# Performance work log

Measured on AMD Instinct MI355X. Metric: run time of the kernel, lower is better.

The kernel has to match this reference:

```python
import jax, jax.numpy as jnp
import numpy as np

B, L, D = 4, 2048, 768
K, M, CK = 12, 1, 4            # heads, thetas, conv kernel size
H = D // (K * M)               # 64
DIM_MEM = K * H                # 768
DIM_EXPAND = H * 3             # 192
DSH = DIM_EXPAND * 2           # 384 swiglu head dim
DST = K * DSH                  # 4608
DIM_FUSED = DIM_MEM + K + DST  # 5388
THETA_MIN, THETA_MAX = 1e-3, 3.0


def setup_inputs() -> dict:
    key = jax.random.key(0)
    ks = jax.random.split(key, 5)
    x = jax.random.normal(ks[0], (B, L, D), jnp.float32)
    W_in = jax.random.normal(ks[1], (D, DIM_FUSED), jnp.float32) * 0.02
    conv_w = jax.random.normal(ks[2], (CK, DIM_MEM + K), jnp.float32) * 0.2  # depthwise taps
    rms_scale = jnp.ones((H,), jnp.float32)
    # theta_raw init (M==1 branch): inverse-sigmoid of geomspace grid
    grid = np.geomspace(THETA_MIN, THETA_MAX, K).reshape(1, 1, K, 1, 1)
    base = np.tile(grid, (1, 1, 1, H, 1))
    u = np.clip((base - THETA_MIN) / (THETA_MAX - THETA_MIN), 1e-4, 1 - 1e-4)
    theta_raw = jnp.asarray(np.log(u) - np.log(1.0 - u), jnp.float32)
    decay_slopes = jnp.asarray(np.log(np.exp(np.geomspace(1e-3, 0.1, K)) - 1.0), jnp.float32)
    score_scale = jnp.ones((K,), jnp.float32)
    tanh_scale = jnp.ones((K,), jnp.float32)
    W_sw = jax.random.normal(ks[3], (2 * K * H * M, DST), jnp.float32) * 0.02
    W_out = jax.random.normal(ks[4], (K * DIM_EXPAND, D), jnp.float32) * 0.02
    return {"x": x, "W_in": W_in, "conv_w": conv_w, "rms_scale": rms_scale,
            "theta_raw": theta_raw, "decay_slopes": decay_slopes,
            "score_scale": score_scale, "tanh_scale": tanh_scale,
            "W_sw": W_sw, "W_out": W_out}


def reference(x, W_in, conv_w, rms_scale, theta_raw, decay_slopes,
              score_scale, tanh_scale, W_sw, W_out):
    # fused in-projection
    z_fused = jnp.einsum('bld,df->blf', x, W_in)
    z_mem = z_fused[..., :DIM_MEM + K]
    skip_direct = z_fused[..., DIM_MEM + K:]
    # causal depthwise conv (kernel size CK, left pad CK-1)
    zp = jnp.pad(z_mem, ((0, 0), (CK - 1, 0), (0, 0)))
    z_conv = sum(zp[:, j:j + L, :] * conv_w[j] for j in range(CK))
    z_mem = jax.nn.silu(z_conv)
    # memory keys + RMSNorm over H
    k_val = z_mem[..., :DIM_MEM].reshape(B, L, K, H)
    k_val = k_val * jax.lax.rsqrt(jnp.mean(k_val * k_val, axis=-1, keepdims=True) + 1e-6) * rms_scale
    s_raw = z_mem[..., DIM_MEM:]  # (B, L, K)
    # theta (M == 1)
    theta = THETA_MIN + (THETA_MAX - THETA_MIN) * jax.nn.sigmoid(theta_raw)  # (1,1,K,H,1)
    # decay time weights (num_anchor_heads == 0, maxlen == L)
    pos = jnp.arange(L, dtype=jnp.float32)
    slopes = jax.nn.softplus(decay_slopes).reshape(1, 1, K)
    dist = jnp.maximum(jnp.float32(L - 1) - pos, 0.0)
    log_time_weight = -slopes * dist[None, :, None]  # (1, L, K)
    log_p = jnp.clip(score_scale[None, None, :] * s_raw, -10.0, 10.0)
    p_w = jnp.exp(log_p + log_time_weight)  # (B, L, K)
    # characteristic-function encoding
    k5 = k_val[..., None]  # (B, L, K, H, 1)
    phi = jnp.tanh(k5 * tanh_scale.reshape(1, 1, K, 1, 1)) * theta
    kvw = k5 * p_w[..., None, None]
    re = kvw * jnp.cos(phi)
    im = kvw * jnp.sin(phi)
    # fused causal cumulative accumulation
    flat = K * H * M
    stack = jnp.concatenate([p_w, re.reshape(B, L, flat), im.reshape(B, L, flat)], axis=-1)
    cs = jnp.cumsum(stack, axis=1)
    den_acc = cs[..., :K]
    re_acc = cs[..., K:K + flat].reshape(B, L, K, H, M)
    im_acc = cs[..., K + flat:].reshape(B, L, K, H, M)
    inv_den = (1.0 / jnp.maximum(den_acc, 1e-4))[..., None, None]
    summary_flat = jnp.stack([re_acc * inv_den, im_acc * inv_den], axis=-1).reshape(B, L, -1)
    # SwiGLU with skip
    y_spectral = jnp.einsum('bls,sf->blf', summary_flat, W_sw).reshape(B, L, K, DSH)
    y_skip = skip_direct.reshape(B, L, K, DSH)
    y_spec_val, y_spec_gate = jnp.split(y_spectral, 2, axis=-1)
    y_skip_val, y_skip_gate = jnp.split(y_skip, 2, axis=-1)
    y_act = (y_spec_val + y_skip_val) * jax.nn.silu(y_spec_gate + y_skip_gate)
    out = jnp.einsum('blf,fd->bld', y_act.reshape(B, L, -1), W_out)
    return out
```

## Files before the change

kernel.cpp:

```cpp
#include <hip/hip_runtime.h>
#include <hip/hip_bf16.h>

#define B_       4
#define L_       2048
#define D_       768
#define K_       12
#define H_       64
#define CK_      4
#define DIM_MEM_ 768
#define DMK      780
#define NT       (B_*L_)
#define NSUM     1536
#define NACT     2304
#define NCHUNK   16
#define CHLEN    (L_/NCHUNK)
#define PSTRIDE  132

typedef __attribute__((ext_vector_type(8))) short          bf16x8;
typedef __attribute__((ext_vector_type(8))) unsigned short u16x8;
typedef __attribute__((ext_vector_type(4))) float          f32x4;

__device__ __forceinline__ ushort f2bf(float v) {
    __hip_bfloat16 h = __float2bfloat16(v);
    return *reinterpret_cast<ushort*>(&h);
}
__device__ __forceinline__ float tanh_fast(float x) {
    float t = __expf(-2.f * fabsf(x));
    float r = (1.f - t) / (1.f + t);
    return copysignf(r, x);
}

struct PrepJobs {
    const float* W[6];
    ushort*      out[6];
    int ldw[6], Kd[6], colbase[6], remap[6], ntx[6];
    int start[7];
    const float* cast_in;
    ushort*      cast_out;
    int n4;
};

__global__ __launch_bounds__(256)
void prep_all(PrepJobs J)
{
    int blk = blockIdx.x;
    if (blk >= J.start[6]) {
        int i = (blk - J.start[6]) * 256 + threadIdx.x;
        if (i < J.n4) {
            float4 v = reinterpret_cast<const float4*>(J.cast_in)[i];
            ushort4 o;
            o.x = f2bf(v.x); o.y = f2bf(v.y); o.z = f2bf(v.z); o.w = f2bf(v.w);
            reinterpret_cast<ushort4*>(J.cast_out)[i] = o;
        }
        return;
    }
    int j = 0;
    while (blk >= J.start[j + 1]) ++j;
    int rel = blk - J.start[j];
    int ntx = J.ntx[j];
    int n0 = (rel % ntx) * 32, k0 = (rel / ntx) * 32;
    const float* W = J.W[j];
    int ldw = J.ldw[j], Kd = J.Kd[j], colbase = J.colbase[j], remap = J.remap[j];
    ushort* out = J.out[j];

    __shared__ float tile[32][33];
    int tx = threadIdx.x & 31, ty = threadIdx.x >> 5;
    int n = n0 + tx;
    int c;
    if (remap) {
        int grp = n >> 5, which = (n >> 4) & 1, nn = (grp << 4) + (n & 15);
        c = colbase + (nn / 192) * 384 + which * 192 + (nn % 192);
    } else {
        c = colbase + n;
    }
    #pragma unroll
    for (int r = 0; r < 4; ++r)
        tile[ty + r*8][tx] = W[(size_t)(k0 + ty + r*8) * ldw + c];
    __syncthreads();
    #pragma unroll
    for (int r = 0; r < 4; ++r)
        out[(size_t)(n0 + ty + r*8) * Kd + k0 + tx] = f2bf(tile[tx][ty + r*8]);
}

__global__ __launch_bounds__(256)
void gemm_bf16_mfma(const ushort* __restrict__ A, const ushort* __restrict__ BT,
                    float* __restrict__ C, int Kd, int N, int ldc)
{
    __shared__ ushort As[128*64];
    __shared__ ushort Bs[128*64];
    int tid = threadIdx.x, lane = tid & 63;
    int lr = lane & 15, quad = lane >> 4;
    int wave = tid >> 6;
    int wr = (wave >> 1) * 64, wc = (wave & 1) * 64;
    int m0 = blockIdx.y * 128, n0 = blockIdx.x * 128;

    f32x4 acc[4][4] = {};

    int srow = tid >> 3;
    int tc   = tid & 7;
    const ushort* gA = A  + (size_t)(m0 + srow) * Kd + tc * 8;
    const ushort* gB = BT + (size_t)(n0 + srow) * Kd + tc * 8;
    int woff = srow * 64 + ((tc ^ (srow & 7)) * 8);
    int rx = lr & 7;

    for (int k0 = 0; k0 < Kd; k0 += 64) {
        u16x8 a[4], b[4];
        #pragma unroll
        for (int p = 0; p < 4; ++p) {
            a[p] = *reinterpret_cast<const u16x8*>(gA + (size_t)(32*p) * Kd);
            b[p] = *reinterpret_cast<const u16x8*>(gB + (size_t)(32*p) * Kd);
        }
        gA += 64; gB += 64;
        __syncthreads();
        #pragma unroll
        for (int p = 0; p < 4; ++p) {
            *reinterpret_cast<u16x8*>(As + woff + p*2048) = a[p];
            *reinterpret_cast<u16x8*>(Bs + woff + p*2048) = b[p];
        }
        __syncthreads();
        #pragma unroll
        for (int ks = 0; ks < 2; ++ks) {
            bf16x8 af[4], bf[4];
            #pragma unroll
            for (int i = 0; i < 4; ++i) {
                int ca = ((ks*4 + quad) ^ rx) * 8;
                af[i] = *reinterpret_cast<const bf16x8*>(As + (wr + i*16 + lr) * 64 + ca);
                bf[i] = *reinterpret_cast<const bf16x8*>(Bs + (wc + i*16 + lr) * 64 + ca);
            }
            #pragma unroll
            for (int i = 0; i < 4; ++i)
                #pragma unroll
                for (int j = 0; j < 4; ++j)
                    acc[i][j] = __builtin_amdgcn_mfma_f32_16x16x32_bf16(
                                    af[i], bf[j], acc[i][j], 0, 0, 0);
        }
    }

    #pragma unroll
    for (int i = 0; i < 4; ++i)
        #pragma unroll
        for (int j = 0; j < 4; ++j)
            #pragma unroll
            for (int r = 0; r < 4; ++r) {
                int row = m0 + wr + i*16 + quad*4 + r;
                int col = n0 + wc + j*16 + lr;
                if (col < N)
                    C[(size_t)row * ldc + col] = acc[i][j][r];
            }
}

#define G2NKT 36

#define GLOAD16(gp, dp) __builtin_amdgcn_global_load_lds( \
    (__attribute__((address_space(1))) const void*)(gp),  \
    (__attribute__((address_space(3))) void*)(dp), 16, 0, 0)

__device__ __forceinline__ void g2_stageA(ushort* lds_, int kt,
                                          const ushort* pAs, const ushort* pAx,
                                          int wave, int part)
{
    int ktc = kt > (G2NKT-1) ? (G2NKT-1) : kt;
    const ushort* g; size_t kd;
    if (ktc < 24) { g = pAs + ktc*64;      kd = 1536; }
    else          { g = pAx + (ktc-24)*64; kd = 768;  }
    g += (size_t)(part * 64) * kd;
    ushort* d = lds_ + (kt & 1) * 8192 + part * 4096 + wave * 512;
    GLOAD16(g,           d);
    GLOAD16(g + 32*kd,   d + 2048);
}

__device__ __forceinline__ void g2_stageB(ushort* lds_, int kt,
                                          const ushort* pBs, const ushort* pBx,
                                          int wave)
{
    int ktc = kt > (G2NKT-1) ? (G2NKT-1) : kt;
    const ushort* g; size_t kd;
    if (ktc < 24) { g = pBs + ktc*64;      kd = 1536; }
    else          { g = pBx + (ktc-24)*64; kd = 768;  }
    ushort* d = lds_ + 16384 + (kt & 1) * 12288 + wave * 512;
    #pragma unroll
    for (int s = 0; s < 6; ++s)
        GLOAD16(g + (size_t)(32*s)*kd, d + 2048*s);
}

__global__ __launch_bounds__(256, 2)
void gemm2_1ph(const ushort* __restrict__ Sm, const ushort* __restrict__ Xb,
               const ushort* __restrict__ WsC, const ushort* __restrict__ WiC,
               ushort* __restrict__ yact)
{
    __shared__ ushort lds[40960];
    const int tid  = threadIdx.x;
    const int lane = tid & 63, wave = tid >> 6;
    const int lr = lane & 15, quad = lane >> 4, rx = lr & 7;
    const int wr = (wave >> 1) * 64;
    const int wc = (wave & 1) * 96;
    const int m0 = blockIdx.y * 128, n0 = blockIdx.x * 192;

    const int sr = tid >> 3;
    const int sc = (tid & 7) ^ (sr & 7);
    const ushort* pAs = Sm  + (size_t)(m0 + sr) * 1536 + sc * 8;
    const ushort* pAx = Xb  + (size_t)(m0 + sr) * 768  + sc * 8;
    const ushort* pBs = WsC + (size_t)(n0 + sr) * 1536 + sc * 8;
    const ushort* pBx = WiC + (size_t)(n0 + sr) * 768  + sc * 8;

    f32x4 acc[4][6] = {};
    const int ca0 = (quad ^ rx) * 8;
    const int ca1 = ((4 + quad) ^ rx) * 8;

    g2_stageA(lds, 0, pAs, pAx, wave, 0);
    g2_stageA(lds, 0, pAs, pAx, wave, 1);
    g2_stageB(lds, 0, pBs, pBx, wave);
    asm volatile("s_waitcnt vmcnt(0)" ::: "memory");
    __builtin_amdgcn_s_barrier();

    #pragma unroll 1
    for (int g = 0; g < G2NKT; ++g) {
        const ushort* Ab = lds + (g & 1) * 8192;
        const ushort* Bb = lds + 16384 + (g & 1) * 12288;

        g2_stageA(lds, g + 1, pAs, pAx, wave, 0);
        g2_stageA(lds, g + 1, pAs, pAx, wave, 1);
        g2_stageB(lds, g + 1, pBs, pBx, wave);

        bf16x8 af[4][2], bfr[6][2];
        #pragma unroll
        for (int i = 0; i < 4; ++i) {
            const ushort* p = Ab + (wr + i*16 + lr) * 64;
            af[i][0] = *reinterpret_cast<const bf16x8*>(p + ca0);
            af[i][1] = *reinterpret_cast<const bf16x8*>(p + ca1);
        }
        #pragma unroll
        for (int j = 0; j < 6; ++j) {
            const ushort* p = Bb + (wc + j*16 + lr) * 64;
            bfr[j][0] = *reinterpret_cast<const bf16x8*>(p + ca0);
            bfr[j][1] = *reinterpret_cast<const bf16x8*>(p + ca1);
        }
        __builtin_amdgcn_s_setprio(1);
        #pragma unroll
        for (int ks = 0; ks < 2; ++ks)
            #pragma unroll
            for (int i = 0; i < 4; ++i)
                #pragma unroll
                for (int j = 0; j < 6; ++j)
                    acc[i][j] = __builtin_amdgcn_mfma_f32_16x16x32_bf16(
                                    af[i][ks], bfr[j][ks], acc[i][j], 0, 0, 0);
        __builtin_amdgcn_s_setprio(0);

        asm volatile("s_waitcnt vmcnt(0)" ::: "memory");
        __builtin_amdgcn_s_barrier();
    }

    const int vg0 = (n0 + wc) >> 5;
    #pragma unroll
    for (int i = 0; i < 4; ++i)
        #pragma unroll
        for (int p = 0; p < 3; ++p)
            #pragma unroll
            for (int r = 0; r < 4; ++r) {
                int row = m0 + wr + i*16 + quad*4 + r;
                int col = (vg0 + p)*16 + lr;
                float v  = acc[i][2*p][r];
                float gt = acc[i][2*p + 1][r];
                float y = v * (gt / (1.f + __expf(-gt)));
                yact[(size_t)row * NACT + col] = f2bf(y);
            }
}

__global__ __launch_bounds__(256)
void token_kernel(const float* __restrict__ zmem, const float* __restrict__ conv_w,
                  const float* __restrict__ rms_scale, const float* __restrict__ theta_raw,
                  const float* __restrict__ dslopes, const float* __restrict__ sscale,
                  const float* __restrict__ tscale,
                  float* __restrict__ pw, float* __restrict__ re, float* __restrict__ im)
{
    int t = blockIdx.x;
    int b = t >> 11;
    int l = t & (L_ - 1);
    int tid = threadIdx.x;
    int h = tid & 63, kg = tid >> 6;

    __shared__ float s_pw[K_];

    if (tid < K_) {
        float acc = 0.f;
        #pragma unroll
        for (int j = 0; j < CK_; ++j) {
            int ll = l - (CK_ - 1) + j;
            if (ll >= 0)
                acc += zmem[(size_t)(b*L_ + ll)*DMK + DIM_MEM_ + tid]
                     * conv_w[j*DMK + DIM_MEM_ + tid];
        }
        float s  = acc / (1.f + expf(-acc));
        float lp = sscale[tid] * s;
        lp = fminf(10.f, fmaxf(-10.f, lp));
        float slope = log1pf(expf(dslopes[tid]));
        s_pw[tid] = expf(lp - slope * (float)(L_ - 1 - l));
    }

    float kv[3];
    #pragma unroll
    for (int q = 0; q < 3; ++q) {
        int kk = kg + q*4;
        int c = kk*H_ + h;
        float acc = 0.f;
        #pragma unroll
        for (int j = 0; j < CK_; ++j) {
            int ll = l - (CK_ - 1) + j;
            if (ll >= 0)
                acc += zmem[(size_t)(b*L_ + ll)*DMK + c] * conv_w[j*DMK + c];
        }
        kv[q] = acc / (1.f + __expf(-acc));
    }
    __syncthreads();

    #pragma unroll
    for (int q = 0; q < 3; ++q) {
        int kk = kg + q*4;
        float v = kv[q];
        float ss = v * v;
        #pragma unroll
        for (int off = 32; off > 0; off >>= 1)
            ss += __shfl_xor(ss, off, 64);
        float kn = v * rsqrtf(ss * (1.f/64.f) + 1e-6f) * rms_scale[h];
        float th = 0.001f + 2.999f * (1.f / (1.f + __expf(-theta_raw[kk*H_ + h])));
        float phi = tanh_fast(kn * tscale[kk]) * th;
        float kvw = kn * s_pw[kk];
        re[(size_t)t*(K_*H_) + kk*H_ + h] = kvw * __cosf(phi);
        im[(size_t)t*(K_*H_) + kk*H_ + h] = kvw * __sinf(phi);
    }
    if (tid < K_) pw[(size_t)t*K_ + tid] = s_pw[tid];
}

__global__ __launch_bounds__(128)
void scan_sums(const float* __restrict__ pw, const float* __restrict__ re,
               const float* __restrict__ im, float* __restrict__ part)
{
    int blk = blockIdx.x;
    int chunk = blk & (NCHUNK - 1);
    int bk = blk >> 4;
    int k = bk % K_;
    int b = bk / K_;
    int tid = threadIdx.x;
    int h = tid & 63;
    const float* __restrict__ src = (tid >> 6) ? im : re;
    int l0 = chunk * CHLEN;

    size_t base  = ((size_t)(b*L_ + l0))*(K_*H_) + k*H_ + h;
    size_t dbase = ((size_t)(b*L_ + l0))*K_ + k;
    float s = 0.f, ds = 0.f;
    for (int i0 = 0; i0 < CHLEN; i0 += 8) {
        float v[8], d[8];
        #pragma unroll
        for (int j = 0; j < 8; ++j) {
            v[j] = src[base + (size_t)(i0 + j)*(K_*H_)];
            d[j] = pw [dbase + (size_t)(i0 + j)*K_];
        }
        #pragma unroll
        for (int j = 0; j < 8; ++j) { s += v[j]; ds += d[j]; }
    }
    size_t pb = ((size_t)bk * NCHUNK + chunk) * PSTRIDE;
    part[pb + tid] = s;
    if (tid == 0) part[pb + 128] = ds;
}

__global__ __launch_bounds__(128)
void scan_final(const float* __restrict__ pw, const float* __restrict__ re,
                const float* __restrict__ im, const float* __restrict__ part,
                ushort* __restrict__ summary)
{
    int blk = blockIdx.x;
    int chunk = blk & (NCHUNK - 1);
    int bk = blk >> 4;
    int k = bk % K_;
    int b = bk / K_;
    int tid = threadIdx.x;
    int h = tid & 63;
    int pi = tid >> 6;
    const float* __restrict__ src = pi ? im : re;
    int l0 = chunk * CHLEN;

    float acc = 0.f, dacc = 0.f;
    size_t pb0 = (size_t)bk * NCHUNK * PSTRIDE;
    for (int cn = 0; cn < chunk; ++cn) {
        acc  += part[pb0 + (size_t)cn*PSTRIDE + tid];
        dacc += part[pb0 + (size_t)cn*PSTRIDE + 128];
    }

    size_t base  = ((size_t)(b*L_ + l0))*(K_*H_) + k*H_ + h;
    size_t dbase = ((size_t)(b*L_ + l0))*K_ + k;
    int outch = 2*(k*H_ + h) + pi;
    for (int i0 = 0; i0 < CHLEN; i0 += 8) {
        float v[8], d[8];
        #pragma unroll
        for (int j = 0; j < 8; ++j) {
            v[j] = src[base + (size_t)(i0 + j)*(K_*H_)];
            d[j] = pw [dbase + (size_t)(i0 + j)*K_];
        }
        #pragma unroll
        for (int j = 0; j < 8; ++j) {
            acc += v[j]; dacc += d[j];
            float inv = 1.f / fmaxf(dacc, 1e-4f);
            summary[((size_t)(b*L_ + l0 + i0 + j))*NSUM + outch] = f2bf(acc * inv);
        }
    }
}

extern "C" void kernel_launch(void* const* d_in, const int* in_sizes, int n_in,
                              void* d_out, int out_size, void* d_ws, size_t ws_size,
                              hipStream_t stream)
{
    const float* x         = (const float*)d_in[0];
    const float* W_in      = (const float*)d_in[1];
    const float* conv_w    = (const float*)d_in[2];
    const float* rms_scale = (const float*)d_in[3];
    const float* theta_raw = (const float*)d_in[4];
    const float* dslopes   = (const float*)d_in[5];
    const float* sscale    = (const float*)d_in[6];
    const float* tscale    = (const float*)d_in[7];
    const float* W_sw      = (const float*)d_in[8];
    const float* W_out     = (const float*)d_in[9];
    float* out = (float*)d_out;
    char* ws   = (char*)d_ws;

    float*  zmem    = (float*) (ws + 0);
    ushort* summary = (ushort*)(ws + 0);
    float*  pw      = (float*) (ws + 25559040);
    float*  re      = (float*) (ws + 25952256);
    float*  im      = (float*) (ws + 51118080);
    ushort* yact    = (ushort*)(ws + 25952256);
    float*  part    = (float*) (ws + 76283904);
    ushort* xb      = (ushort*)(ws + 76689408);
    ushort* WiCat   = (ushort*)(ws + 89272320);
    ushort* WsCat   = (ushort*)(ws + 96350208);
    ushort* WoT     = (ushort*)(ws + 110505984);
    ushort* WimT    = (ushort*)(ws + 114044928);

    PrepJobs J{};
    J.W[0]=W_in;  J.out[0]=WiCat; J.ldw[0]=5388; J.Kd[0]=768;  J.colbase[0]=780; J.remap[0]=1; J.ntx[0]=144;
    J.W[1]=W_sw;  J.out[1]=WsCat; J.ldw[1]=4608; J.Kd[1]=1536; J.colbase[1]=0;   J.remap[1]=1; J.ntx[1]=144;
    J.W[2]=W_out; J.out[2]=WoT;   J.ldw[2]=768;  J.Kd[2]=2304; J.colbase[2]=0;   J.remap[2]=0; J.ntx[2]=24;
    J.W[3]=W_in;  J.out[3]=WimT;  J.ldw[3]=5388; J.Kd[3]=768;  J.colbase[3]=0;   J.remap[3]=0; J.ntx[3]=28;
    int tiles[4] = {144*24, 144*48, 24*72, 28*24};
    J.start[0] = 0;
    for (int j = 0; j < 4; ++j) J.start[j+1] = J.start[j] + tiles[j];
    J.start[5] = J.start[4];
    J.start[6] = J.start[4];
    J.cast_in = x; J.cast_out = xb; J.n4 = NT*D_/4;
    int nblk = J.start[6] + (J.n4 + 255)/256;

    dim3 blk(256);
    prep_all<<<dim3(nblk), blk, 0, stream>>>(J);
    gemm_bf16_mfma<<<dim3(7, 64), blk, 0, stream>>>(xb, WimT, zmem, 768, 780, 780);
    token_kernel<<<dim3(NT), blk, 0, stream>>>(zmem, conv_w, rms_scale, theta_raw,
                                               dslopes, sscale, tscale, pw, re, im);
    scan_sums <<<dim3(B_*K_*NCHUNK), dim3(128), 0, stream>>>(pw, re, im, part);
    scan_final<<<dim3(B_*K_*NCHUNK), dim3(128), 0, stream>>>(pw, re, im, part, summary);
    gemm2_1ph<<<dim3(24, 64), dim3(256), 0, stream>>>(summary, xb, WsCat, WiCat, yact);
    gemm_bf16_mfma<<<dim3(6, 64), blk, 0, stream>>>(yact, WoT, out, 2304, 768, 768);
}
```

Before: 418.3 us.

## Load GEMM2 A operand directly into registers, staging only B through LDS

The second GEMM no longer stages the A tile (summary/x rows) through shared memory. Each wave loads its own A fragments straight from global memory into double-buffered registers one k-step ahead, and only B goes through LDS via global_load_lds. The loop is unrolled by two with alternating register buffers, and the wait only drains the B LDS loads (vmcnt(8)), so the A register loads stay in flight. This shrinks LDS from 80KB to 48KB and removes the A LDS reads, at the cost of more VGPRs and less coalesced global reads, since each lane reads 16 bytes from separate rows.

```diff
diff --git a/kernel.cpp b/kernel.cpp
--- a/kernel.cpp
+++ b/kernel.cpp
@@ -149,46 +149,58 @@
             }
 }
 
-#define G2NKT 36
-
 #define GLOAD16(gp, dp) __builtin_amdgcn_global_load_lds( \
     (__attribute__((address_space(1))) const void*)(gp),  \
     (__attribute__((address_space(3))) void*)(dp), 16, 0, 0)
 
-__device__ __forceinline__ void g2_stageA(ushort* lds_, int kt,
-                                          const ushort* pAs, const ushort* pAx,
-                                          int wave, int part)
-{
-    int ktc = kt > (G2NKT-1) ? (G2NKT-1) : kt;
-    const ushort* g; size_t kd;
-    if (ktc < 24) { g = pAs + ktc*64;      kd = 1536; }
-    else          { g = pAx + (ktc-24)*64; kd = 768;  }
-    g += (size_t)(part * 64) * kd;
-    ushort* d = lds_ + (kt & 1) * 8192 + part * 4096 + wave * 512;
-    GLOAD16(g,           d);
-    GLOAD16(g + 32*kd,   d + 2048);
-}
-
-__device__ __forceinline__ void g2_stageB(ushort* lds_, int kt,
-                                          const ushort* pBs, const ushort* pBx,
-                                          int wave)
-{
-    int ktc = kt > (G2NKT-1) ? (G2NKT-1) : kt;
-    const ushort* g; size_t kd;
-    if (ktc < 24) { g = pBs + ktc*64;      kd = 1536; }
-    else          { g = pBx + (ktc-24)*64; kd = 768;  }
-    ushort* d = lds_ + 16384 + (kt & 1) * 12288 + wave * 512;
-    #pragma unroll
-    for (int s = 0; s < 6; ++s)
-        GLOAD16(g + (size_t)(32*s)*kd, d + 2048*s);
-}
+#define G2BODY(AF_USE, AF_LD, PAR, PREF, PA_NEXT, KDA, PB_NEXT, KDB)          \
+  do {                                                                        \
+    if (PREF) {                                                               \
+        ushort* bd = lds + ((PAR)^1)*12288 + wave*512;                        \
+        const ushort* bsrc = (PB_NEXT);                                       \
+        _Pragma("unroll")                                                     \
+        for (int s = 0; s < 6; ++s)                                           \
+            GLOAD16(bsrc + (size_t)(32*s)*(KDB), bd + 2048*s);                \
+        __builtin_amdgcn_sched_barrier(0);   \
+        const ushort* asrc = (PA_NEXT);                                       \
+        _Pragma("unroll")                                                     \
+        for (int i = 0; i < 4; ++i) {                                         \
+            AF_LD[i][0] = *reinterpret_cast<const bf16x8*>(                   \
+                              asrc + (size_t)(i*16)*(KDA));                   \
+            AF_LD[i][1] = *reinterpret_cast<const bf16x8*>(                   \
+                              asrc + (size_t)(i*16)*(KDA) + 32);              \
+        }                                                                     \
+    }                                                                         \
+    const ushort* Bb = lds + (PAR)*12288;                                     \
+    bf16x8 bfr[6][2];                                                         \
+    _Pragma("unroll")                                                         \
+    for (int j = 0; j < 6; ++j) {                                             \
+        const ushort* p = Bb + (wc + j*16 + lr) * 64;                         \
+        bfr[j][0] = *reinterpret_cast<const bf16x8*>(p + ca0);                \
+        bfr[j][1] = *reinterpret_cast<const bf16x8*>(p + ca1);                \
+    }                                                                         \
+    __builtin_amdgcn_s_setprio(1);                                            \
+    _Pragma("unroll")                                                         \
+    for (int ks = 0; ks < 2; ++ks)                                            \
+        _Pragma("unroll")                                                     \
+        for (int i = 0; i < 4; ++i)                                           \
+            _Pragma("unroll")                                                 \
+            for (int j = 0; j < 6; ++j)                                       \
+                acc[i][j] = __builtin_amdgcn_mfma_f32_16x16x32_bf16(          \
+                                AF_USE[i][ks], bfr[j][ks], acc[i][j], 0,0,0); \
+    __builtin_amdgcn_s_setprio(0);                                            \
+    if (PREF) {                                                               \
+        asm volatile("s_waitcnt vmcnt(8)" ::: "memory");                      \
+        __builtin_amdgcn_s_barrier();                                         \
+    }                                                                         \
+  } while (0)
 
 __global__ __launch_bounds__(256, 2)
-void gemm2_1ph(const ushort* __restrict__ Sm, const ushort* __restrict__ Xb,
-               const ushort* __restrict__ WsC, const ushort* __restrict__ WiC,
-               ushort* __restrict__ yact)
-{
-    __shared__ ushort lds[40960];
+void gemm2_areg(const ushort* __restrict__ Sm, const ushort* __restrict__ Xb,
+                const ushort* __restrict__ WsC, const ushort* __restrict__ WiC,
+                ushort* __restrict__ yact)
+{
+    __shared__ ushort lds[24576];
     const int tid  = threadIdx.x;
     const int lane = tid & 63, wave = tid >> 6;
     const int lr = lane & 15, quad = lane >> 4, rx = lr & 7;
@@ -198,57 +210,46 @@
 
     const int sr = tid >> 3;
     const int sc = (tid & 7) ^ (sr & 7);
-    const ushort* pAs = Sm  + (size_t)(m0 + sr) * 1536 + sc * 8;
-    const ushort* pAx = Xb  + (size_t)(m0 + sr) * 768  + sc * 8;
-    const ushort* pBs = WsC + (size_t)(n0 + sr) * 1536 + sc * 8;
-    const ushort* pBx = WiC + (size_t)(n0 + sr) * 768  + sc * 8;
+    const ushort* pB1 = WsC + (size_t)(n0 + sr) * 1536 + sc * 8;
+    const ushort* pB2 = WiC + (size_t)(n0 + sr) * 768  + sc * 8;
+
+    const ushort* pA1 = Sm + (size_t)(m0 + wr + lr) * 1536 + quad * 8;
+    const ushort* pA2 = Xb + (size_t)(m0 + wr + lr) * 768  + quad * 8;
 
     f32x4 acc[4][6] = {};
+    bf16x8 af0[4][2], af1[4][2];
     const int ca0 = (quad ^ rx) * 8;
     const int ca1 = ((4 + quad) ^ rx) * 8;
 
-    g2_stageA(lds, 0, pAs, pAx, wave, 0);
-    g2_stageA(lds, 0, pAs, pAx, wave, 1);
-    g2_stageB(lds, 0, pBs, pBx, wave);
-    asm volatile("s_waitcnt vmcnt(0)" ::: "memory");
-    __builtin_amdgcn_s_barrier();
+    {
+        ushort* bd = lds + wave*512;
+        #pragma unroll
+        for (int s = 0; s < 6; ++s)
+            GLOAD16(pB1 + (size_t)(32*s)*1536, bd + 2048*s);
+        __builtin_amdgcn_sched_barrier(0);
+        #pragma unroll
+        for (int i = 0; i < 4; ++i) {
+            af0[i][0] = *reinterpret_cast<const bf16x8*>(pA1 + (size_t)(i*16)*1536);
+            af0[i][1] = *reinterpret_cast<const bf16x8*>(pA1 + (size_t)(i*16)*1536 + 32);
+        }
+        asm volatile("s_waitcnt vmcnt(8)" ::: "memory");
+        __builtin_amdgcn_s_barrier();
+    }
 
     #pragma unroll 1
-    for (int g = 0; g < G2NKT; ++g) {
-        const ushort* Ab = lds + (g & 1) * 8192;
-        const ushort* Bb = lds + 16384 + (g & 1) * 12288;
-
-        g2_stageA(lds, g + 1, pAs, pAx, wave, 0);
-        g2_stageA(lds, g + 1, pAs, pAx, wave, 1);
-        g2_stageB(lds, g + 1, pBs, pBx, wave);
-
-        bf16x8 af[4][2], bfr[6][2];
-        #pragma unroll
-        for (int i = 0; i < 4; ++i) {
-            const ushort* p = Ab + (wr + i*16 + lr) * 64;
-            af[i][0] = *reinterpret_cast<const bf16x8*>(p + ca0);
-            af[i][1] = *reinterpret_cast<const bf16x8*>(p + ca1);
-        }
-        #pragma unroll
-        for (int j = 0; j < 6; ++j) {
-            const ushort* p = Bb + (wc + j*16 + lr) * 64;
-            bfr[j][0] = *reinterpret_cast<const bf16x8*>(p + ca0);
-            bfr[j][1] = *reinterpret_cast<const bf16x8*>(p + ca1);
-        }
-        __builtin_amdgcn_s_setprio(1);
-        #pragma unroll
-        for (int ks = 0; ks < 2; ++ks)
-            #pragma unroll
-            for (int i = 0; i < 4; ++i)
-                #pragma unroll
-                for (int j = 0; j < 6; ++j)
-                    acc[i][j] = __builtin_amdgcn_mfma_f32_16x16x32_bf16(
-                                    af[i][ks], bfr[j][ks], acc[i][j], 0, 0, 0);
-        __builtin_amdgcn_s_setprio(0);
-
-        asm volatile("s_waitcnt vmcnt(0)" ::: "memory");
-        __builtin_amdgcn_s_barrier();
-    }
+    for (int t = 0; t < 22; t += 2) {
+        G2BODY(af0, af1, 0, true, pA1 + (t+1)*64, 1536, pB1 + (t+1)*64, 1536);
+        G2BODY(af1, af0, 1, true, pA1 + (t+2)*64, 1536, pB1 + (t+2)*64, 1536);
+    }
+    G2BODY(af0, af1, 0, true, pA1 + 23*64, 1536, pB1 + 23*64, 1536);
+    G2BODY(af1, af0, 1, true, pA2,          768, pB2,          768);
+    #pragma unroll 1
+    for (int t = 0; t < 10; t += 2) {
+        G2BODY(af0, af1, 0, true, pA2 + (t+1)*64, 768, pB2 + (t+1)*64, 768);
+        G2BODY(af1, af0, 1, true, pA2 + (t+2)*64, 768, pB2 + (t+2)*64, 768);
+    }
+    G2BODY(af0, af1, 0, true,  pA2 + 11*64, 768, pB2 + 11*64, 768);
+    G2BODY(af1, af0, 1, false, pA2,         768, pB2,         768);
 
     const int vg0 = (n0 + wc) >> 5;
     #pragma unroll
@@ -455,6 +456,6 @@
                                                dslopes, sscale, tscale, pw, re, im);
     scan_sums <<<dim3(B_*K_*NCHUNK), dim3(128), 0, stream>>>(pw, re, im, part);
     scan_final<<<dim3(B_*K_*NCHUNK), dim3(128), 0, stream>>>(pw, re, im, part, summary);
-    gemm2_1ph<<<dim3(24, 64), dim3(256), 0, stream>>>(summary, xb, WsCat, WiCat, yact);
+    gemm2_areg<<<dim3(24, 64), dim3(256), 0, stream>>>(summary, xb, WsCat, WiCat, yact);
     gemm_bf16_mfma<<<dim3(6, 64), blk, 0, stream>>>(yact, WoT, out, 2304, 768, 768);
 }
```

After: 534.5 us. +27.8%, slower.

## Fuse token feature computation into chunk-sum scan kernel with chunk-major layout

Applied to the files above, without the earlier changes.

Merges the per-token conv/RMSNorm/encoding kernel with the first scan pass, so each block walks its chunk sequentially with a rolling conv window, writes re/im/pw in a chunk-contiguous layout and produces the chunk partial sums in the same pass. The goal is to drop one kernel launch and a full re-read of the re/im/pw intermediates, and to make the final scan's reads contiguous. The cost is much less parallelism: 768 blocks of 128 threads that each loop sequentially over 64 tokens, with a wave shuffle reduction per token, in place of 8192 wide blocks.

```diff
diff --git a/kernel.cpp b/kernel.cpp
--- a/kernel.cpp
+++ b/kernel.cpp
@@ -266,74 +266,13 @@
             }
 }
 
-__global__ __launch_bounds__(256)
-void token_kernel(const float* __restrict__ zmem, const float* __restrict__ conv_w,
-                  const float* __restrict__ rms_scale, const float* __restrict__ theta_raw,
-                  const float* __restrict__ dslopes, const float* __restrict__ sscale,
-                  const float* __restrict__ tscale,
-                  float* __restrict__ pw, float* __restrict__ re, float* __restrict__ im)
-{
-    int t = blockIdx.x;
-    int b = t >> 11;
-    int l = t & (L_ - 1);
-    int tid = threadIdx.x;
-    int h = tid & 63, kg = tid >> 6;
-
-    __shared__ float s_pw[K_];
-
-    if (tid < K_) {
-        float acc = 0.f;
-        #pragma unroll
-        for (int j = 0; j < CK_; ++j) {
-            int ll = l - (CK_ - 1) + j;
-            if (ll >= 0)
-                acc += zmem[(size_t)(b*L_ + ll)*DMK + DIM_MEM_ + tid]
-                     * conv_w[j*DMK + DIM_MEM_ + tid];
-        }
-        float s  = acc / (1.f + expf(-acc));
-        float lp = sscale[tid] * s;
-        lp = fminf(10.f, fmaxf(-10.f, lp));
-        float slope = log1pf(expf(dslopes[tid]));
-        s_pw[tid] = expf(lp - slope * (float)(L_ - 1 - l));
-    }
-
-    float kv[3];
-    #pragma unroll
-    for (int q = 0; q < 3; ++q) {
-        int kk = kg + q*4;
-        int c = kk*H_ + h;
-        float acc = 0.f;
-        #pragma unroll
-        for (int j = 0; j < CK_; ++j) {
-            int ll = l - (CK_ - 1) + j;
-            if (ll >= 0)
-                acc += zmem[(size_t)(b*L_ + ll)*DMK + c] * conv_w[j*DMK + c];
-        }
-        kv[q] = acc / (1.f + __expf(-acc));
-    }
-    __syncthreads();
-
-    #pragma unroll
-    for (int q = 0; q < 3; ++q) {
-        int kk = kg + q*4;
-        float v = kv[q];
-        float ss = v * v;
-        #pragma unroll
-        for (int off = 32; off > 0; off >>= 1)
-            ss += __shfl_xor(ss, off, 64);
-        float kn = v * rsqrtf(ss * (1.f/64.f) + 1e-6f) * rms_scale[h];
-        float th = 0.001f + 2.999f * (1.f / (1.f + __expf(-theta_raw[kk*H_ + h])));
-        float phi = tanh_fast(kn * tscale[kk]) * th;
-        float kvw = kn * s_pw[kk];
-        re[(size_t)t*(K_*H_) + kk*H_ + h] = kvw * __cosf(phi);
-        im[(size_t)t*(K_*H_) + kk*H_ + h] = kvw * __sinf(phi);
-    }
-    if (tid < K_) pw[(size_t)t*K_ + tid] = s_pw[tid];
-}
-
 __global__ __launch_bounds__(128)
-void scan_sums(const float* __restrict__ pw, const float* __restrict__ re,
-               const float* __restrict__ im, float* __restrict__ part)
+void token_scan1(const float* __restrict__ zmem, const float* __restrict__ conv_w,
+                 const float* __restrict__ rms_scale, const float* __restrict__ theta_raw,
+                 const float* __restrict__ dslopes, const float* __restrict__ sscale,
+                 const float* __restrict__ tscale,
+                 float* __restrict__ reN, float* __restrict__ imN,
+                 float* __restrict__ pwN, float* __restrict__ part)
 {
     int blk = blockIdx.x;
     int chunk = blk & (NCHUNK - 1);
@@ -342,31 +281,88 @@
     int b = bk / K_;
     int tid = threadIdx.x;
     int h = tid & 63;
-    const float* __restrict__ src = (tid >> 6) ? im : re;
-    int l0 = chunk * CHLEN;
-
-    size_t base  = ((size_t)(b*L_ + l0))*(K_*H_) + k*H_ + h;
-    size_t dbase = ((size_t)(b*L_ + l0))*K_ + k;
-    float s = 0.f, ds = 0.f;
-    for (int i0 = 0; i0 < CHLEN; i0 += 8) {
-        float v[8], d[8];
+    int tt = tid >> 6;
+    int l0 = chunk * CHLEN + tt * 64;
+
+    int c  = k*H_ + h;
+    int cs = DIM_MEM_ + k;
+
+    float cw0 = conv_w[0*DMK + c], cw1 = conv_w[1*DMK + c];
+    float cw2 = conv_w[2*DMK + c], cw3 = conv_w[3*DMK + c];
+    float cs0 = conv_w[0*DMK + cs], cs1 = conv_w[1*DMK + cs];
+    float cs2 = conv_w[2*DMK + cs], cs3 = conv_w[3*DMK + cs];
+    float rs  = rms_scale[h];
+    float th  = 0.001f + 2.999f * (1.f / (1.f + __expf(-theta_raw[c])));
+    float ts  = tscale[k];
+    float scl = sscale[k];
+    float slope = log1pf(expf(dslopes[k]));
+
+    const float* zb = zmem + (size_t)(b*L_) * DMK;
+
+    float z3=0.f, z2=0.f, z1=0.f, s3=0.f, s2=0.f, s1=0.f;
+    {
+        int ll = l0 - 3;
+        if (ll >= 0)     { z3 = zb[(size_t)ll*DMK + c];     s3 = zb[(size_t)ll*DMK + cs]; }
+        if (ll + 1 >= 0) { z2 = zb[(size_t)(ll+1)*DMK + c]; s2 = zb[(size_t)(ll+1)*DMK + cs]; }
+        if (ll + 2 >= 0) { z1 = zb[(size_t)(ll+2)*DMK + c]; s1 = zb[(size_t)(ll+2)*DMK + cs]; }
+    }
+
+    float sre = 0.f, sim = 0.f, spw = 0.f;
+    size_t obase = (size_t)blk * (CHLEN*H_) + (size_t)(tt*64)*H_ + h;
+
+    for (int i0 = 0; i0 < 64; i0 += 8) {
+        float zl[8], sl[8];
         #pragma unroll
         for (int j = 0; j < 8; ++j) {
-            v[j] = src[base + (size_t)(i0 + j)*(K_*H_)];
-            d[j] = pw [dbase + (size_t)(i0 + j)*K_];
-        }
-        #pragma unroll
-        for (int j = 0; j < 8; ++j) { s += v[j]; ds += d[j]; }
-    }
-    size_t pb = ((size_t)bk * NCHUNK + chunk) * PSTRIDE;
-    part[pb + tid] = s;
-    if (tid == 0) part[pb + 128] = ds;
+            int l = l0 + i0 + j;
+            zl[j] = zb[(size_t)l*DMK + c];
+            sl[j] = zb[(size_t)l*DMK + cs];
+        }
+        #pragma unroll
+        for (int j = 0; j < 8; ++j) {
+            int l = l0 + i0 + j;
+            float a3 = zl[j], b3 = sl[j];
+            float acc  = cw0*z3 + cw1*z2 + cw2*z1 + cw3*a3;
+            float acc2 = cs0*s3 + cs1*s2 + cs2*s1 + cs3*b3;
+            z3 = z2; z2 = z1; z1 = a3;
+            s3 = s2; s2 = s1; s1 = b3;
+
+            float kv = acc / (1.f + __expf(-acc));
+            float ss = kv * kv;
+            #pragma unroll
+            for (int off = 32; off > 0; off >>= 1)
+                ss += __shfl_xor(ss, off, 64);
+            float kn  = kv * rsqrtf(ss * (1.f/64.f) + 1e-6f) * rs;
+            float phi = tanh_fast(kn * ts) * th;
+
+            float s  = acc2 / (1.f + expf(-acc2));
+            float lp = fminf(10.f, fmaxf(-10.f, scl * s));
+            float pwv = expf(lp - slope * (float)(L_ - 1 - l));
+
+            float kvw = kn * pwv;
+            float rev = kvw * __cosf(phi);
+            float imv = kvw * __sinf(phi);
+            reN[obase + (size_t)(i0 + j)*H_] = rev;
+            imN[obase + (size_t)(i0 + j)*H_] = imv;
+            sre += rev; sim += imv; spw += pwv;
+            if (h == 0) pwN[(size_t)bk * L_ + l] = pwv;
+        }
+    }
+
+    __shared__ float red[2][64], imd[2][64], pwd[2];
+    red[tt][h] = sre; imd[tt][h] = sim;
+    if (h == 0) pwd[tt] = spw;
+    __syncthreads();
+    size_t pb = (size_t)blk * PSTRIDE;
+    if (tid < 64) part[pb + tid] = red[0][tid] + red[1][tid];
+    else          part[pb + tid] = imd[0][tid - 64] + imd[1][tid - 64];
+    if (tid == 0) part[pb + 128] = pwd[0] + pwd[1];
 }
 
 __global__ __launch_bounds__(128)
-void scan_final(const float* __restrict__ pw, const float* __restrict__ re,
-                const float* __restrict__ im, const float* __restrict__ part,
-                ushort* __restrict__ summary)
+void scan_final2(const float* __restrict__ pwN, const float* __restrict__ reN,
+                 const float* __restrict__ imN, const float* __restrict__ part,
+                 ushort* __restrict__ summary)
 {
     int blk = blockIdx.x;
     int chunk = blk & (NCHUNK - 1);
@@ -376,25 +372,25 @@
     int tid = threadIdx.x;
     int h = tid & 63;
     int pi = tid >> 6;
-    const float* __restrict__ src = pi ? im : re;
+    const float* __restrict__ src = pi ? imN : reN;
     int l0 = chunk * CHLEN;
 
     float acc = 0.f, dacc = 0.f;
-    size_t pb0 = (size_t)bk * NCHUNK * PSTRIDE;
+    size_t pb0 = (size_t)(bk * NCHUNK) * PSTRIDE;
     for (int cn = 0; cn < chunk; ++cn) {
         acc  += part[pb0 + (size_t)cn*PSTRIDE + tid];
         dacc += part[pb0 + (size_t)cn*PSTRIDE + 128];
     }
 
-    size_t base  = ((size_t)(b*L_ + l0))*(K_*H_) + k*H_ + h;
-    size_t dbase = ((size_t)(b*L_ + l0))*K_ + k;
+    size_t base  = (size_t)blk * (CHLEN*H_) + h;
+    size_t dbase = (size_t)bk * L_ + l0;
     int outch = 2*(k*H_ + h) + pi;
     for (int i0 = 0; i0 < CHLEN; i0 += 8) {
         float v[8], d[8];
         #pragma unroll
         for (int j = 0; j < 8; ++j) {
-            v[j] = src[base + (size_t)(i0 + j)*(K_*H_)];
-            d[j] = pw [dbase + (size_t)(i0 + j)*K_];
+            v[j] = src[base + (size_t)(i0 + j)*H_];
+            d[j] = pwN[dbase + i0 + j];
         }
         #pragma unroll
         for (int j = 0; j < 8; ++j) {
@@ -451,10 +447,10 @@
     dim3 blk(256);
     prep_all<<<dim3(nblk), blk, 0, stream>>>(J);
     gemm_bf16_mfma<<<dim3(7, 64), blk, 0, stream>>>(xb, WimT, zmem, 768, 780, 780);
-    token_kernel<<<dim3(NT), blk, 0, stream>>>(zmem, conv_w, rms_scale, theta_raw,
-                                               dslopes, sscale, tscale, pw, re, im);
-    scan_sums <<<dim3(B_*K_*NCHUNK), dim3(128), 0, stream>>>(pw, re, im, part);
-    scan_final<<<dim3(B_*K_*NCHUNK), dim3(128), 0, stream>>>(pw, re, im, part, summary);
+    token_scan1<<<dim3(B_*K_*NCHUNK), dim3(128), 0, stream>>>(
+        zmem, conv_w, rms_scale, theta_raw, dslopes, sscale, tscale,
+        re, im, pw, part);
+    scan_final2<<<dim3(B_*K_*NCHUNK), dim3(128), 0, stream>>>(pw, re, im, part, summary);
     gemm2_1ph<<<dim3(24, 64), dim3(256), 0, stream>>>(summary, xb, WsCat, WiCat, yact);
     gemm_bf16_mfma<<<dim3(6, 64), blk, 0, stream>>>(yact, WoT, out, 2304, 768, 768);
 }
```

Result: faster. 399.3 us (-4.5%).
